# Performance work log

Measured on AMD Instinct MI355X. Metric: run time of the kernel, lower is better.

Reference implementation:

```python
import jax, jax.numpy as jnp
import numpy as np

N = 4096     # batch of positions
E = 32       # descriptor buckets (experts)
NBLK = 12    # residual blocks per head


def _ln(x, g, b, eps=1e-5):
    m = x.mean(-1, keepdims=True)
    v = ((x - m) ** 2).mean(-1, keepdims=True)
    return (x - m) / jnp.sqrt(v + eps) * g + b


def _gelu(x):
    return jax.nn.gelu(x, approximate=False)  # torch nn.GELU default = exact erf


def setup_inputs() -> dict:
    key = jax.random.key(0)
    ks = iter(jax.random.split(key, 64))

    def nrm(shape, scale=0.05):
        return jax.random.normal(next(ks), shape, jnp.float32) * scale

    return {
        "piece_idx": jax.random.randint(next(ks), (N, 64), 0, 12),
        "side_flag": jax.random.randint(next(ks), (N,), 0, 2),
        "ep_file": jax.random.randint(next(ks), (N,), 0, 8),
        "castle_ms": jax.random.uniform(next(ks), (N, 4), jnp.float32),
        "fifty_a": jax.random.uniform(next(ks), (N,), jnp.float32),
        "descriptor_index": jax.random.randint(next(ks), (N,), 0, E),
        # per-bucket embedding tables, stacked on a leading expert axis
        "Wp_w": nrm((E, 64, 12, 32)), "Wp_b": nrm((E, 64, 12, 32)),
        "Wc_w": nrm((E, 4, 32)), "Wc_b": nrm((E, 4, 32)),
        "Wep_w": nrm((E, 8, 32)), "Wep_b": nrm((E, 8, 32)),
        "Wf_w": nrm((E, 2, 32)), "Wf_b": nrm((E, 2, 32)),
        # per-bucket MLP head params (weights stored as [in,out])
        "fc1_w": nrm((E, 2240, 256)), "fc1_b": nrm((E, 256)),
        "ln1_g": jnp.ones((E, 256)), "ln1_b": jnp.zeros((E, 256)),
        "fc2_w": nrm((E, 256, 32)), "fc2_b": nrm((E, 32)),
        "ln2_g": jnp.ones((E, 32)), "ln2_b": jnp.zeros((E, 32)),
        "blkA_w": nrm((NBLK, E, 32, 32)), "blkA_b": nrm((NBLK, E, 32)),
        "blkA_g": jnp.ones((NBLK, E, 32)), "blkA_be": jnp.zeros((NBLK, E, 32)),
        "blkB_w": nrm((NBLK, E, 32, 32)), "blkB_b": nrm((NBLK, E, 32)),
        "blkB_g": jnp.ones((NBLK, E, 32)), "blkB_be": jnp.zeros((NBLK, E, 32)),
        "out_w": nrm((E, 32, 51)), "out_b": nrm((E, 51)),
        "bins": jnp.linspace(0.0, 1.0, 51),
    }


def reference(piece_idx, side_flag, ep_file, castle_ms, fifty_a, descriptor_index,
              Wp_w, Wp_b, Wc_w, Wc_b, Wep_w, Wep_b, Wf_w, Wf_b,
              fc1_w, fc1_b, ln1_g, ln1_b, fc2_w, fc2_b, ln2_g, ln2_b,
              blkA_w, blkA_b, blkA_g, blkA_be, blkB_w, blkB_b, blkB_g, blkB_be,
              out_w, out_b, bins):
    desc = descriptor_index
    side = side_flag.astype(bool)
    n = piece_idx.shape[0]

    # ---- per-bucket, side-selected embedding gathers -> x_emb [N,2240] ----
    sq = jnp.arange(64)
    pc = jnp.maximum(piece_idx, 0)                                 # clamp -1 -> 0
    w_emb = Wp_w[desc[:, None], sq[None, :], pc]                    # [N,64,32]
    b_emb = Wp_b[desc[:, None], sq[None, :], pc]
    piece_emb = jnp.where(side[:, None, None], b_emb, w_emb)
    piece_emb = piece_emb * (piece_idx >= 0)[..., None].astype(piece_emb.dtype)
    pieces_vec = piece_emb.reshape(n, 2048)

    Wc = jnp.where(side[:, None, None], Wc_b[desc], Wc_w[desc])     # [N,4,32]
    castle_vec = (castle_ms[..., None] * Wc).reshape(n, 128)

    Wep = jnp.where(side[:, None, None], Wep_b[desc], Wep_w[desc])  # [N,8,32]
    epc = jnp.maximum(ep_file, 0)
    ep_vec = jnp.take_along_axis(Wep, epc[:, None, None], axis=1)[:, 0]
    ep_vec = ep_vec * (ep_file >= 0)[:, None].astype(ep_vec.dtype)

    Wf = jnp.where(side[:, None, None], Wf_b[desc], Wf_w[desc])     # [N,2,32]
    fifty_vec = (1.0 - fifty_a)[:, None] * Wf[:, 0] + fifty_a[:, None] * Wf[:, 1]

    x = jnp.concatenate([pieces_vec, castle_vec, ep_vec, fifty_vec], axis=1)  # [N,2240]

    # ---- expert-routed dense layer: all-expert GEMM + per-token select ----
    def dense_moe(h, W, b):
        ha = jnp.einsum('nd,edh->neh', h, W)                        # [N,E,out]
        hsel = jnp.take_along_axis(ha, desc[:, None, None], axis=1)[:, 0]
        return hsel + b[desc]

    h = _ln(_gelu(dense_moe(x, fc1_w, fc1_b)), ln1_g[desc], ln1_b[desc])   # [N,256]
    h = _ln(_gelu(dense_moe(h, fc2_w, fc2_b)), ln2_g[desc], ln2_b[desc])   # [N,32]

    def blk(carry, p):
        wA, bA, gA, beA, wB, bB, gB, beB = p
        y = _ln(_gelu(dense_moe(carry, wA, bA)), gA[desc], beA[desc])
        y = _ln(_gelu(dense_moe(y, wB, bB)), gB[desc], beB[desc])
        return carry + y, None

    h, _ = jax.lax.scan(blk, h, (blkA_w, blkA_b, blkA_g, blkA_be,
                                 blkB_w, blkB_b, blkB_g, blkB_be))

    logits = dense_moe(_gelu(h), out_w, out_b)                      # [N,51]
    p_win = jnp.sum(jax.nn.softmax(logits, axis=-1) * bins, axis=-1, keepdims=True)
    return logits, p_win
```

## Files before the change

### kernel.cpp

```cpp
#include <hip/hip_runtime.h>
#include <math.h>

#define N 4096
#define E 32
#define NBLK 12
#define D_IN 2240
#define H1 256
#define H2 32
#define NOUT 51
#define MT 16
#define NPAD (N + E*(MT-1))
#define NTILE (NPAD/MT)
#define KSPLIT 4
#define NROWS 4608
#define GMAX 96
#define NCONVBLK (35*4*E)

typedef short s8v __attribute__((ext_vector_type(8)));
typedef float f4v __attribute__((ext_vector_type(4)));

__device__ __forceinline__ float gelu(float x){
    return 0.5f * x * (1.0f + erff(x * 0.70710678118654752f));
}
__device__ __forceinline__ unsigned short f2bf(float f){
    unsigned int u = __float_as_uint(f);
    unsigned int r = (u + 0x7fffu + ((u >> 16) & 1u)) >> 16;
    return (unsigned short)r;
}

__global__ void k_sort(const int* __restrict__ desc,
                       int* __restrict__ perm, int* __restrict__ tile_e,
                       int4* __restrict__ garr, int* __restrict__ ngroups){
    __shared__ int scnt[E];
    __shared__ int spoff[E+1];
    __shared__ int scur[E];
    int tid = threadIdx.x;
    if (tid < E) scnt[tid] = 0;
    __syncthreads();
    for (int n = tid; n < N; n += blockDim.x) atomicAdd(&scnt[desc[n]], 1);
    __syncthreads();
    if (tid == 0){
        int run = 0;
        for (int e = 0; e < E; e++){ spoff[e] = run; run += ((scnt[e] + MT - 1)/MT)*MT; }
        spoff[E] = run;
        int ng = 0;
        for (int e = 0; e < E; e++){
            int t0 = spoff[e]/MT, t1 = spoff[e+1]/MT;
            for (int t = t0; t < t1; t += 8){
                int nv = t1 - t; if (nv > 8) nv = 8;
                if (ng < GMAX) garr[ng] = make_int4(t, e, nv, 0);
                ng++;
            }
        }
        *ngroups = (ng > GMAX) ? GMAX : ng;
    }
    __syncthreads();
    if (tid < E) scur[tid] = spoff[tid];
    for (int p = tid; p < NPAD; p += blockDim.x) perm[p] = -1;
    __syncthreads();
    for (int n = tid; n < N; n += blockDim.x){
        int p = atomicAdd(&scur[desc[n]], 1);
        perm[p] = n;
    }
    for (int t = tid; t < NTILE; t += blockDim.x){
        int p0 = t*MT;
        int e = -1;
        if (p0 < spoff[E]){
            for (int q = 0; q < E; q++){
                if (p0 >= spoff[q] && p0 < spoff[q+1]){ e = q; break; }
            }
        }
        tile_e[t] = e;
    }
}

__global__ void k_prep(const int* __restrict__ perm,
                       const int* __restrict__ piece_idx,
                       const int* __restrict__ side_flag,
                       const int* __restrict__ ep_file,
                       const float* __restrict__ castle_ms,
                       const float* __restrict__ fifty_a,
                       const int* __restrict__ desc_idx,
                       const float* __restrict__ Wp_w, const float* __restrict__ Wp_b,
                       const float* __restrict__ Wc_w, const float* __restrict__ Wc_b,
                       const float* __restrict__ Wep_w, const float* __restrict__ Wep_b,
                       const float* __restrict__ Wf_w, const float* __restrict__ Wf_b,
                       unsigned short* __restrict__ xs,
                       const float* __restrict__ W1, unsigned short* __restrict__ Wt){
    __shared__ float lds[64][65];
    int tid = threadIdx.x;
    if (blockIdx.x >= NPAD){
        int b = blockIdx.x - NPAD;
        int kt = b % 35;
        int nt = (b / 35) & 3;
        int e  = b / 140;
        int k0 = kt*64, n0 = nt*64;
        int kk = tid >> 4, nn = (tid & 15) * 4;
        const float* src = W1 + ((size_t)e*D_IN + k0)*H1 + n0;
        #pragma unroll
        for (int r = 0; r < 4; r++){
            float4 v = *(const float4*)(src + (size_t)(kk + r*16)*H1 + nn);
            lds[kk + r*16][nn]   = v.x;
            lds[kk + r*16][nn+1] = v.y;
            lds[kk + r*16][nn+2] = v.z;
            lds[kk + r*16][nn+3] = v.w;
        }
        __syncthreads();
        int n = tid >> 2, kq = tid & 3;
        s8v p0, p1;
        #pragma unroll
        for (int j = 0; j < 8; j++) p0[j] = (short)f2bf(lds[kq*16 + j][n]);
        #pragma unroll
        for (int j = 0; j < 8; j++) p1[j] = (short)f2bf(lds[kq*16 + 8 + j][n]);
        unsigned short* dst = Wt + ((size_t)(e*H1 + n0 + n))*D_IN + k0 + kq*16;
        *(s8v*)dst       = p0;
        *(s8v*)(dst + 8) = p1;
        return;
    }
    int pos = blockIdx.x;
    int row = perm[pos];
    unsigned short* xr = xs + (size_t)pos * D_IN;
    if (row < 0){
        s8v z = {0,0,0,0,0,0,0,0};
        for (int t = tid; t < D_IN/8; t += blockDim.x) *(s8v*)(xr + t*8) = z;
        return;
    }
    int d = desc_idx[row];
    int s = side_flag[row];
    __shared__ int pidx[64];
    if (tid < 64) pidx[tid] = piece_idx[row*64 + tid];
    __syncthreads();
    const float* Wp  = s ? Wp_b  : Wp_w;
    const float* Wc  = s ? Wc_b  : Wc_w;
    const float* Wep = s ? Wep_b : Wep_w;
    const float* Wf  = s ? Wf_b  : Wf_w;
    int ep  = ep_file[row];
    int epc = ep > 0 ? ep : 0;
    float a = fifty_a[row];
    for (int t = tid; t < D_IN/8; t += blockDim.x){
        int i0 = t*8;
        float v[8];
        if (i0 < 2048){
            int sq = i0 >> 5, c0 = i0 & 31;
            int pc = pidx[sq];
            float msk = pc >= 0 ? 1.0f : 0.0f;
            int pcc = pc > 0 ? pc : 0;
            const float* base = Wp + (((size_t)d*64 + sq)*12 + pcc)*32 + c0;
            float4 a0 = *(const float4*)base;
            float4 a1 = *(const float4*)(base + 4);
            v[0]=a0.x*msk; v[1]=a0.y*msk; v[2]=a0.z*msk; v[3]=a0.w*msk;
            v[4]=a1.x*msk; v[5]=a1.y*msk; v[6]=a1.z*msk; v[7]=a1.w*msk;
        } else if (i0 < 2176){
            int j = i0 - 2048; int ci = j >> 5, c0 = j & 31;
            float cv = castle_ms[row*4 + ci];
            const float* base = Wc + ((size_t)d*4 + ci)*32 + c0;
            float4 a0 = *(const float4*)base;
            float4 a1 = *(const float4*)(base + 4);
            v[0]=a0.x*cv; v[1]=a0.y*cv; v[2]=a0.z*cv; v[3]=a0.w*cv;
            v[4]=a1.x*cv; v[5]=a1.y*cv; v[6]=a1.z*cv; v[7]=a1.w*cv;
        } else if (i0 < 2208){
            int c0 = i0 - 2176;
            float msk = ep >= 0 ? 1.0f : 0.0f;
            const float* base = Wep + ((size_t)d*8 + epc)*32 + c0;
            float4 a0 = *(const float4*)base;
            float4 a1 = *(const float4*)(base + 4);
            v[0]=a0.x*msk; v[1]=a0.y*msk; v[2]=a0.z*msk; v[3]=a0.w*msk;
            v[4]=a1.x*msk; v[5]=a1.y*msk; v[6]=a1.z*msk; v[7]=a1.w*msk;
        } else {
            int c0 = i0 - 2208;
            #pragma unroll
            for (int j = 0; j < 8; j++)
                v[j] = (1.0f - a) * Wf[(size_t)d*64 + c0 + j] + a * Wf[(size_t)d*64 + 32 + c0 + j];
        }
        s8v p;
        #pragma unroll
        for (int j = 0; j < 8; j++) p[j] = (short)f2bf(v[j]);
        *(s8v*)(xr + i0) = p;
    }
}

__launch_bounds__(256)
__global__ void k_fc1(const int4* __restrict__ garr, const int* __restrict__ ngroups,
                      const unsigned short* __restrict__ xs,
                      const unsigned short* __restrict__ Wt,
                      float* __restrict__ h1p){
    int g = blockIdx.x;
    if (g >= *ngroups) return;
    int4 gi = garr[g];
    int tile0 = gi.x, e = gi.y, nv = gi.z;
    int kc = blockIdx.y, nh = blockIdx.z;
    int kstart = (kc <= 2) ? kc*18 : 53;
    int nsteps = (kc < 2) ? 18 : 17;
    int lane = threadIdx.x & 63, wave = threadIdx.x >> 6;
    int quad = lane >> 4, l16 = lane & 15;
    int col0 = nh*128 + wave*32 + l16;
    const unsigned short* Ab = xs + (size_t)(tile0*MT + l16)*D_IN + quad*8;
    const unsigned short* B0 = Wt + ((size_t)e*H1 + col0)*D_IN + quad*8;
    const unsigned short* B1 = B0 + (size_t)16*D_IN;
    f4v acc[8][2];
    #pragma unroll
    for (int mt = 0; mt < 8; mt++){ acc[mt][0] = (f4v){0.f,0.f,0.f,0.f}; acc[mt][1] = (f4v){0.f,0.f,0.f,0.f}; }
    int kend = kstart + nsteps;
    #pragma unroll 2
    for (int s = kstart; s < kend; s++){
        int ko = s*32;
        s8v b0 = *(const s8v*)(B0 + ko);
        s8v b1 = *(const s8v*)(B1 + ko);
        #pragma unroll
        for (int mt = 0; mt < 8; mt++){
            s8v av = *(const s8v*)(Ab + (size_t)mt*MT*D_IN + ko);
            acc[mt][0] = __builtin_amdgcn_mfma_f32_16x16x32_bf16(av, b0, acc[mt][0], 0, 0, 0);
            acc[mt][1] = __builtin_amdgcn_mfma_f32_16x16x32_bf16(av, b1, acc[mt][1], 0, 0, 0);
        }
    }
    float* out = h1p + (size_t)kc*NROWS*H1;
    #pragma unroll
    for (int mt = 0; mt < 8; mt++){
        if (mt >= nv) break;
        int posb = (tile0 + mt)*MT + quad*4;
        #pragma unroll
        for (int r = 0; r < 4; r++){
            out[(size_t)(posb + r)*H1 + col0]      = acc[mt][0][r];
            out[(size_t)(posb + r)*H1 + col0 + 16] = acc[mt][1][r];
        }
    }
}

__launch_bounds__(512)
__global__ void k_tail(const int* __restrict__ tile_e, const int* __restrict__ perm,
                       const float* __restrict__ h1p, const float* __restrict__ b1,
                       const float* __restrict__ g1, const float* __restrict__ be1,
                       const float* __restrict__ W2, const float* __restrict__ b2,
                       const float* __restrict__ g2, const float* __restrict__ be2,
                       const float* __restrict__ Aw, const float* __restrict__ Abv,
                       const float* __restrict__ Ag, const float* __restrict__ Abe,
                       const float* __restrict__ Bw, const float* __restrict__ Bb,
                       const float* __restrict__ Bg, const float* __restrict__ Bbe,
                       const float* __restrict__ Ow, const float* __restrict__ Ob,
                       const float* __restrict__ bins,
                       float* __restrict__ out){
    int t = blockIdx.x;
    int e = tile_e[t];
    if (e < 0) return;
    int tid = threadIdx.x;

    __shared__ __align__(16) float sh[MT][260];
    __shared__ __align__(16) float sh2[MT][36];
    __shared__ __align__(16) float sh3[MT][36];
    __shared__ __align__(16) float smem_u[8192];

    {
        const float* W2e = W2 + (size_t)e*H1*H2;
        for (int i = tid; i < H1*H2; i += 512){
            int k = i >> 5, c = i & 31;
            smem_u[((k>>2)*32 + c)*4 + (k&3)] = W2e[i];
        }
    }
    for (int slot = tid; slot < MT*64; slot += 512){
        int r = slot >> 6, c4 = (slot & 63) << 2;
        int row = t*MT + r;
        float4 v = {0.f,0.f,0.f,0.f};
        #pragma unroll
        for (int kc = 0; kc < KSPLIT; kc++){
            float4 p = *(const float4*)(h1p + ((size_t)kc*NROWS + row)*H1 + c4);
            v.x += p.x; v.y += p.y; v.z += p.z; v.w += p.w;
        }
        float4 bb = *(const float4*)(b1 + e*H1 + c4);
        sh[r][c4]   = gelu(v.x + bb.x);
        sh[r][c4+1] = gelu(v.y + bb.y);
        sh[r][c4+2] = gelu(v.z + bb.z);
        sh[r][c4+3] = gelu(v.w + bb.w);
    }
    __syncthreads();

    int m = tid >> 5, c = tid & 31;
    {
        float s = 0.f;
        #pragma unroll
        for (int j = 0; j < 8; j++) s += sh[m][c + 32*j];
        #pragma unroll
        for (int o = 16; o > 0; o >>= 1) s += __shfl_xor(s, o);
        float mean = s * (1.0f/H1);
        float v2 = 0.f;
        #pragma unroll
        for (int j = 0; j < 8; j++){ float d = sh[m][c + 32*j] - mean; v2 += d*d; }
        #pragma unroll
        for (int o = 16; o > 0; o >>= 1) v2 += __shfl_xor(v2, o);
        float rs = rsqrtf(v2 * (1.0f/H1) + 1e-5f);
        #pragma unroll
        for (int j = 0; j < 8; j++){
            int k = c + 32*j;
            sh[m][k] = (sh[m][k] - mean) * rs * g1[e*H1 + k] + be1[e*H1 + k];
        }
    }
    float hv;
    {
        const float4* W2T = (const float4*)smem_u;
        float q0=0.f,q1=0.f,q2=0.f,q3=0.f;
        #pragma unroll 8
        for (int j = 0; j < 64; j++){
            float4 h4 = *(const float4*)&sh[m][j*4];
            float4 w4 = W2T[j*32 + c];
            q0 = fmaf(h4.x, w4.x, q0);
            q1 = fmaf(h4.y, w4.y, q1);
            q2 = fmaf(h4.z, w4.z, q2);
            q3 = fmaf(h4.w, w4.w, q3);
        }
        float acc = (q0+q1) + (q2+q3) + b2[e*H2 + c];
        float y = gelu(acc);
        float ss = y;
        #pragma unroll
        for (int o = 16; o > 0; o >>= 1) ss += __shfl_xor(ss, o);
        float mean2 = ss * (1.0f/H2);
        float dv = y - mean2;
        float vv = dv*dv;
        #pragma unroll
        for (int o = 16; o > 0; o >>= 1) vv += __shfl_xor(vv, o);
        hv = dv * rsqrtf(vv*(1.0f/H2) + 1e-5f) * g2[e*H2+c] + be2[e*H2+c];
    }
    __syncthreads();

    float* ATf = smem_u;
    float* BTf = smem_u + 2048;
    const float4* AT4 = (const float4*)ATf;
    const float4* BT4 = (const float4*)BTf;

    for (int tb = 0; tb < NBLK; tb++){
        size_t wb = (size_t)tb*E + e;
        const float* A = Aw + wb*1024;
        const float* B = Bw + wb*1024;
        int p = tb & 1;
        for (int i = tid; i < 1024; i += 512){
            int k = i >> 5, cc = i & 31;
            int off = (p*256 + (k>>2)*32 + cc)*4 + (k&3);
            ATf[off] = A[i];
            BTf[off] = B[i];
        }
        __syncthreads();
        sh2[m][c] = hv;
        float q0=0.f,q1=0.f,q2=0.f,q3=0.f;
        #pragma unroll
        for (int j = 0; j < 8; j++){
            float4 h4 = *(const float4*)&sh2[m][j*4];
            float4 w4 = AT4[p*256 + j*32 + c];
            q0 = fmaf(h4.x, w4.x, q0);
            q1 = fmaf(h4.y, w4.y, q1);
            q2 = fmaf(h4.z, w4.z, q2);
            q3 = fmaf(h4.w, w4.w, q3);
        }
        float ya = (q0+q1) + (q2+q3) + Abv[wb*32 + c];
        ya = gelu(ya);
        float sa = ya;
        #pragma unroll
        for (int o = 16; o > 0; o >>= 1) sa += __shfl_xor(sa, o);
        float ma = sa * (1.0f/H2);
        float da = ya - ma;
        float va = da*da;
        #pragma unroll
        for (int o = 16; o > 0; o >>= 1) va += __shfl_xor(va, o);
        float yA = da * rsqrtf(va*(1.0f/H2) + 1e-5f) * Ag[wb*32+c] + Abe[wb*32+c];
        sh3[m][c] = yA;
        q0=0.f; q1=0.f; q2=0.f; q3=0.f;
        #pragma unroll
        for (int j = 0; j < 8; j++){
            float4 h4 = *(const float4*)&sh3[m][j*4];
            float4 w4 = BT4[p*256 + j*32 + c];
            q0 = fmaf(h4.x, w4.x, q0);
            q1 = fmaf(h4.y, w4.y, q1);
            q2 = fmaf(h4.z, w4.z, q2);
            q3 = fmaf(h4.w, w4.w, q3);
        }
        float yb = (q0+q1) + (q2+q3) + Bb[wb*32 + c];
        yb = gelu(yb);
        float sb2 = yb;
        #pragma unroll
        for (int o = 16; o > 0; o >>= 1) sb2 += __shfl_xor(sb2, o);
        float mb = sb2 * (1.0f/H2);
        float db = yb - mb;
        float vb = db*db;
        #pragma unroll
        for (int o = 16; o > 0; o >>= 1) vb += __shfl_xor(vb, o);
        hv += db * rsqrtf(vb*(1.0f/H2) + 1e-5f) * Bg[wb*32+c] + Bbe[wb*32+c];
    }

    sh2[m][c] = gelu(hv);
    __syncthreads();
    int wave = tid >> 6, lane = tid & 63;
    const float* W = Ow + (size_t)e*32*NOUT;
    for (int rr = wave; rr < MT; rr += 8){
        int orow = perm[t*MT + rr];
        if (orow < 0) continue;
        float acc = (lane < NOUT) ? Ob[e*NOUT + lane] : -INFINITY;
        #pragma unroll
        for (int k = 0; k < 32; k++){
            float gk = sh2[rr][k];
            if (lane < NOUT) acc = fmaf(gk, W[k*NOUT + lane], acc);
        }
        if (lane < NOUT) out[(size_t)orow*NOUT + lane] = acc;
        float mx = acc;
        #pragma unroll
        for (int o = 32; o > 0; o >>= 1) mx = fmaxf(mx, __shfl_xor(mx, o));
        float pp = (lane < NOUT) ? expf(acc - mx) : 0.0f;
        float sum = pp;
        #pragma unroll
        for (int o = 32; o > 0; o >>= 1) sum += __shfl_xor(sum, o);
        float pb = (lane < NOUT) ? pp * bins[lane] : 0.0f;
        float sb = pb;
        #pragma unroll
        for (int o = 32; o > 0; o >>= 1) sb += __shfl_xor(sb, o);
        if (lane == 0) out[(size_t)N*NOUT + orow] = sb / sum;
    }
}

extern "C" void kernel_launch(void* const* d_in, const int* in_sizes, int n_in,
                              void* d_out, int out_size, void* d_ws, size_t ws_size,
                              hipStream_t stream){
    const int*   piece_idx = (const int*)d_in[0];
    const int*   side_flag = (const int*)d_in[1];
    const int*   ep_file   = (const int*)d_in[2];
    const float* castle_ms = (const float*)d_in[3];
    const float* fifty_a   = (const float*)d_in[4];
    const int*   desc      = (const int*)d_in[5];
    const float* Wp_w  = (const float*)d_in[6];
    const float* Wp_b  = (const float*)d_in[7];
    const float* Wc_w  = (const float*)d_in[8];
    const float* Wc_b  = (const float*)d_in[9];
    const float* Wep_w = (const float*)d_in[10];
    const float* Wep_b = (const float*)d_in[11];
    const float* Wf_w  = (const float*)d_in[12];
    const float* Wf_b  = (const float*)d_in[13];
    const float* fc1_w = (const float*)d_in[14];
    const float* fc1_b = (const float*)d_in[15];
    const float* ln1_g = (const float*)d_in[16];
    const float* ln1_b = (const float*)d_in[17];
    const float* fc2_w = (const float*)d_in[18];
    const float* fc2_b = (const float*)d_in[19];
    const float* ln2_g = (const float*)d_in[20];
    const float* ln2_b = (const float*)d_in[21];
    const float* blkA_w  = (const float*)d_in[22];
    const float* blkA_b  = (const float*)d_in[23];
    const float* blkA_g  = (const float*)d_in[24];
    const float* blkA_be = (const float*)d_in[25];
    const float* blkB_w  = (const float*)d_in[26];
    const float* blkB_b  = (const float*)d_in[27];
    const float* blkB_g  = (const float*)d_in[28];
    const float* blkB_be = (const float*)d_in[29];
    const float* out_w = (const float*)d_in[30];
    const float* out_b = (const float*)d_in[31];
    const float* bins  = (const float*)d_in[32];

    char* wsp = (char*)d_ws;
    auto alloc = [&](size_t bytes){ void* p = (void*)wsp; wsp += (bytes + 255) & ~(size_t)255; return p; };
    int*            perm    = (int*)            alloc((size_t)NPAD*4);
    int*            tile_e  = (int*)            alloc((size_t)NTILE*4);
    int4*           garr    = (int4*)           alloc((size_t)GMAX*16);
    int*            ngroups = (int*)            alloc(256);
    unsigned short* Wt      = (unsigned short*) alloc((size_t)E*H1*D_IN*2);
    unsigned short* xs      = (unsigned short*) alloc((size_t)(NPAD+128)*D_IN*2);
    float*          h1p     = (float*)          alloc((size_t)KSPLIT*NROWS*H1*4);

    k_sort<<<1, 256, 0, stream>>>(desc, perm, tile_e, garr, ngroups);
    k_prep<<<NPAD + NCONVBLK, 256, 0, stream>>>(perm, piece_idx, side_flag, ep_file,
                                                castle_ms, fifty_a, desc,
                                                Wp_w, Wp_b, Wc_w, Wc_b,
                                                Wep_w, Wep_b, Wf_w, Wf_b,
                                                xs, fc1_w, Wt);
    k_fc1<<<dim3(GMAX, KSPLIT, 2), 256, 0, stream>>>(garr, ngroups, xs, Wt, h1p);
    k_tail<<<NTILE, 512, 0, stream>>>(tile_e, perm, h1p, fc1_b, ln1_g, ln1_b,
                                      fc2_w, fc2_b, ln2_g, ln2_b,
                                      blkA_w, blkA_b, blkA_g, blkA_be,
                                      blkB_w, blkB_b, blkB_g, blkB_be,
                                      out_w, out_b, bins, (float*)d_out);
}
```

Measured before the change: 314.2 us.

## Preload all residual-block weights as packed bf16 in shared memory upfront

The tail kernel now converts fc2 and all 12 residual-block A/B weight matrices to packed bf16 pairs and stages them in shared memory in one pass before the block loop. It also preloads all per-block bias, gamma and beta vectors into shared memory. This removes the per-iteration weight staging and its loads inside the sequential 12-block loop, and halves the shared-memory footprint of the weights. In exchange, weights are rounded to bf16, which lowers accuracy, and the per-block shared-memory usage grows, which may reduce occupancy.

```diff
diff --git a/kernel.cpp b/kernel.cpp
--- a/kernel.cpp
+++ b/kernel.cpp
@@ -27,6 +27,8 @@
     unsigned int r = (u + 0x7fffu + ((u >> 16) & 1u)) >> 16;
     return (unsigned short)r;
 }
+__device__ __forceinline__ float bflo(unsigned int u){ return __uint_as_float(u << 16); }
+__device__ __forceinline__ float bfhi(unsigned int u){ return __uint_as_float(u & 0xffff0000u); }
 
 __global__ void k_sort(const int* __restrict__ desc,
                        int* __restrict__ perm, int* __restrict__ tile_e,
@@ -244,17 +246,31 @@
     if (e < 0) return;
     int tid = threadIdx.x;
 
-    __shared__ __align__(16) float sh[MT][260];
+    __shared__ __align__(16) unsigned int smem[12288];
+    __shared__ __align__(16) float vecs[NBLK*6*32];
     __shared__ __align__(16) float sh2[MT][36];
     __shared__ __align__(16) float sh3[MT][36];
-    __shared__ __align__(16) float smem_u[8192];
+
+    float* shf = (float*)smem;
+    unsigned int* W2pk = smem + 4160;
 
     {
         const float* W2e = W2 + (size_t)e*H1*H2;
-        for (int i = tid; i < H1*H2; i += 512){
-            int k = i >> 5, c = i & 31;
-            smem_u[((k>>2)*32 + c)*4 + (k&3)] = W2e[i];
-        }
+        for (int j = tid; j < 4096; j += 512){
+            int h = j & 1, q = j >> 1, cc = q & 31, p2 = q >> 5;
+            int k0 = 4*p2 + 2*h;
+            unsigned int lo = f2bf(W2e[k0*32 + cc]);
+            unsigned int hi = f2bf(W2e[(k0+1)*32 + cc]);
+            W2pk[(p2*32 + cc)*2 + h] = lo | (hi << 16);
+        }
+    }
+    for (int j = tid; j < NBLK*6*32; j += 512){
+        int cc = j & 31, vi = (j >> 5) % 6, tb = j / 192;
+        size_t wb = (size_t)tb*E + e;
+        const float* src;
+        switch(vi){ case 0: src=Abv; break; case 1: src=Ag; break; case 2: src=Abe; break;
+                    case 3: src=Bb;  break; case 4: src=Bg; break; default: src=Bbe; }
+        vecs[j] = src[wb*32 + cc];
     }
     for (int slot = tid; slot < MT*64; slot += 512){
         int r = slot >> 6, c4 = (slot & 63) << 2;
@@ -266,10 +282,10 @@
             v.x += p.x; v.y += p.y; v.z += p.z; v.w += p.w;
         }
         float4 bb = *(const float4*)(b1 + e*H1 + c4);
-        sh[r][c4]   = gelu(v.x + bb.x);
-        sh[r][c4+1] = gelu(v.y + bb.y);
-        sh[r][c4+2] = gelu(v.z + bb.z);
-        sh[r][c4+3] = gelu(v.w + bb.w);
+        float4 g4;
+        g4.x = gelu(v.x + bb.x); g4.y = gelu(v.y + bb.y);
+        g4.z = gelu(v.z + bb.z); g4.w = gelu(v.w + bb.w);
+        *(float4*)(shf + r*260 + c4) = g4;
     }
     __syncthreads();
 
@@ -277,34 +293,34 @@
     {
         float s = 0.f;
         #pragma unroll
-        for (int j = 0; j < 8; j++) s += sh[m][c + 32*j];
+        for (int j = 0; j < 8; j++) s += shf[m*260 + c + 32*j];
         #pragma unroll
         for (int o = 16; o > 0; o >>= 1) s += __shfl_xor(s, o);
         float mean = s * (1.0f/H1);
         float v2 = 0.f;
         #pragma unroll
-        for (int j = 0; j < 8; j++){ float d = sh[m][c + 32*j] - mean; v2 += d*d; }
+        for (int j = 0; j < 8; j++){ float d = shf[m*260 + c + 32*j] - mean; v2 += d*d; }
         #pragma unroll
         for (int o = 16; o > 0; o >>= 1) v2 += __shfl_xor(v2, o);
         float rs = rsqrtf(v2 * (1.0f/H1) + 1e-5f);
         #pragma unroll
         for (int j = 0; j < 8; j++){
             int k = c + 32*j;
-            sh[m][k] = (sh[m][k] - mean) * rs * g1[e*H1 + k] + be1[e*H1 + k];
+            shf[m*260 + k] = (shf[m*260 + k] - mean) * rs * g1[e*H1 + k] + be1[e*H1 + k];
         }
     }
     float hv;
     {
-        const float4* W2T = (const float4*)smem_u;
+        const uint2* W2p = (const uint2*)W2pk;
         float q0=0.f,q1=0.f,q2=0.f,q3=0.f;
         #pragma unroll 8
-        for (int j = 0; j < 64; j++){
-            float4 h4 = *(const float4*)&sh[m][j*4];
-            float4 w4 = W2T[j*32 + c];
-            q0 = fmaf(h4.x, w4.x, q0);
-            q1 = fmaf(h4.y, w4.y, q1);
-            q2 = fmaf(h4.z, w4.z, q2);
-            q3 = fmaf(h4.w, w4.w, q3);
+        for (int p2 = 0; p2 < 64; p2++){
+            uint2 w = W2p[p2*32 + c];
+            float4 h4 = *(const float4*)(shf + m*260 + p2*4);
+            q0 = fmaf(h4.x, bflo(w.x), q0);
+            q1 = fmaf(h4.y, bfhi(w.x), q1);
+            q2 = fmaf(h4.z, bflo(w.y), q2);
+            q3 = fmaf(h4.w, bfhi(w.y), q3);
         }
         float acc = (q0+q1) + (q2+q3) + b2[e*H2 + c];
         float y = gelu(acc);
@@ -320,35 +336,34 @@
     }
     __syncthreads();
 
-    float* ATf = smem_u;
-    float* BTf = smem_u + 2048;
-    const float4* AT4 = (const float4*)ATf;
-    const float4* BT4 = (const float4*)BTf;
+    for (int j = tid; j < 12288; j += 512){
+        int tbsub = j >> 9, r = j & 511;
+        int h = r & 1, q = r >> 1, cc = q & 31, p2 = q >> 5;
+        int k0 = 4*p2 + 2*h;
+        const float* src = (tbsub & 1) ? Bw : Aw;
+        size_t base = ((size_t)(tbsub >> 1)*E + e)*1024;
+        unsigned int lo = f2bf(src[base + k0*32 + cc]);
+        unsigned int hi = f2bf(src[base + (k0+1)*32 + cc]);
+        smem[j] = lo | (hi << 16);
+    }
+    __syncthreads();
 
     for (int tb = 0; tb < NBLK; tb++){
-        size_t wb = (size_t)tb*E + e;
-        const float* A = Aw + wb*1024;
-        const float* B = Bw + wb*1024;
-        int p = tb & 1;
-        for (int i = tid; i < 1024; i += 512){
-            int k = i >> 5, cc = i & 31;
-            int off = (p*256 + (k>>2)*32 + cc)*4 + (k&3);
-            ATf[off] = A[i];
-            BTf[off] = B[i];
-        }
-        __syncthreads();
+        const float* vA = &vecs[tb*192];
+        const uint2* WA = (const uint2*)(smem + (tb*2+0)*512);
+        const uint2* WB = (const uint2*)(smem + (tb*2+1)*512);
         sh2[m][c] = hv;
         float q0=0.f,q1=0.f,q2=0.f,q3=0.f;
         #pragma unroll
-        for (int j = 0; j < 8; j++){
-            float4 h4 = *(const float4*)&sh2[m][j*4];
-            float4 w4 = AT4[p*256 + j*32 + c];
-            q0 = fmaf(h4.x, w4.x, q0);
-            q1 = fmaf(h4.y, w4.y, q1);
-            q2 = fmaf(h4.z, w4.z, q2);
-            q3 = fmaf(h4.w, w4.w, q3);
-        }
-        float ya = (q0+q1) + (q2+q3) + Abv[wb*32 + c];
+        for (int p2 = 0; p2 < 8; p2++){
+            uint2 w = WA[p2*32 + c];
+            float4 h4 = *(const float4*)(&sh2[m][p2*4]);
+            q0 = fmaf(h4.x, bflo(w.x), q0);
+            q1 = fmaf(h4.y, bfhi(w.x), q1);
+            q2 = fmaf(h4.z, bflo(w.y), q2);
+            q3 = fmaf(h4.w, bfhi(w.y), q3);
+        }
+        float ya = (q0+q1) + (q2+q3) + vA[c];
         ya = gelu(ya);
         float sa = ya;
         #pragma unroll
@@ -358,19 +373,19 @@
         float va = da*da;
         #pragma unroll
         for (int o = 16; o > 0; o >>= 1) va += __shfl_xor(va, o);
-        float yA = da * rsqrtf(va*(1.0f/H2) + 1e-5f) * Ag[wb*32+c] + Abe[wb*32+c];
+        float yA = da * rsqrtf(va*(1.0f/H2) + 1e-5f) * vA[32+c] + vA[64+c];
         sh3[m][c] = yA;
         q0=0.f; q1=0.f; q2=0.f; q3=0.f;
         #pragma unroll
-        for (int j = 0; j < 8; j++){
-            float4 h4 = *(const float4*)&sh3[m][j*4];
-            float4 w4 = BT4[p*256 + j*32 + c];
-            q0 = fmaf(h4.x, w4.x, q0);
-            q1 = fmaf(h4.y, w4.y, q1);
-            q2 = fmaf(h4.z, w4.z, q2);
-            q3 = fmaf(h4.w, w4.w, q3);
-        }
-        float yb = (q0+q1) + (q2+q3) + Bb[wb*32 + c];
+        for (int p2 = 0; p2 < 8; p2++){
+            uint2 w = WB[p2*32 + c];
+            float4 h4 = *(const float4*)(&sh3[m][p2*4]);
+            q0 = fmaf(h4.x, bflo(w.x), q0);
+            q1 = fmaf(h4.y, bfhi(w.x), q1);
+            q2 = fmaf(h4.z, bflo(w.y), q2);
+            q3 = fmaf(h4.w, bfhi(w.y), q3);
+        }
+        float yb = (q0+q1) + (q2+q3) + vA[96+c];
         yb = gelu(yb);
         float sb2 = yb;
         #pragma unroll
@@ -380,7 +395,7 @@
         float vb = db*db;
         #pragma unroll
         for (int o = 16; o > 0; o >>= 1) vb += __shfl_xor(vb, o);
-        hv += db * rsqrtf(vb*(1.0f/H2) + 1e-5f) * Bg[wb*32+c] + Bbe[wb*32+c];
+        hv += db * rsqrtf(vb*(1.0f/H2) + 1e-5f) * vA[128+c] + vA[160+c];
     }
 
     sh2[m][c] = gelu(hv);
```

After: 312.2 us. No clear change (-0.6%).
